# Kernel optimization log

Hardware: AMD Instinct MI355X
Metric: run time of the kernel (lower is better)

Reference implementation:

```python
import jax, jax.numpy as jnp
import numpy as np

H = 8          # num_heads
T = 2          # num_edge_types
NEG_SLOPE = 0.2


def _edge_softmax(scores, dst, num_nodes):
    # softmax over incoming edges of each destination node, per head
    m = jax.ops.segment_max(scores, dst, num_segments=num_nodes)  # [N,H]
    e = jnp.exp(scores - m[dst])                                   # [E,H]
    s = jax.ops.segment_sum(e, dst, num_segments=num_nodes)        # [N,H]
    return e / s[dst]


def setup_inputs() -> dict:
    key = jax.random.key(0)
    ks = jax.random.split(key, 8)
    N, D, E = 50000, 128, 800000
    return {
        "x": jax.random.normal(ks[0], (N, D), dtype=jnp.float32),
        "w_u": jax.random.normal(ks[1], (H * T, D), dtype=jnp.float32) * (1.0 / np.sqrt(D)),
        "b_u": jax.random.normal(ks[2], (H * T,), dtype=jnp.float32) * 0.01,
        "w_v": jax.random.normal(ks[3], (H * T, D), dtype=jnp.float32) * (1.0 / np.sqrt(D)),
        "src_e0": jax.random.randint(ks[4], (E,), 0, N, dtype=jnp.int32),
        "dst_e0": jax.random.randint(ks[5], (E,), 0, N, dtype=jnp.int32),
        "src_e1": jax.random.randint(ks[6], (E,), 0, N, dtype=jnp.int32),
        "dst_e1": jax.random.randint(ks[7], (E,), 0, N, dtype=jnp.int32),
    }


def reference(x, w_u, b_u, w_v, src_e0, dst_e0, src_e1, dst_e1):
    N, D = x.shape
    head_dim = D // H
    scores_u = x @ w_u.T + b_u   # [N, H*T]
    scores_v = x @ w_v.T         # [N, H*T]
    xh = x.reshape(N, head_dim, H)  # matches torch reshape(-1, head_dim, num_heads)
    outs = [x]  # sep=True
    for t, (src, dst) in enumerate([(src_e0, dst_e0), (src_e1, dst_e1)]):
        u = scores_u[:, t * H:(t + 1) * H]
        v = scores_v[:, t * H:(t + 1) * H]
        s = u[src] + v[dst]                         # u_add_v -> [E,H]
        s = jnp.where(s >= 0, s, NEG_SLOPE * s)     # LeakyReLU(0.2)
        p = _edge_softmax(s, dst, N)                # [E,H]
        msg = xh[src] * p[:, None, :]               # u_mul_e -> [E,head_dim,H]
        agg = jax.ops.segment_sum(msg, dst, num_segments=N)  # [N,head_dim,H]
        outs.append(agg.reshape(N, D))
    return jnp.concatenate(outs, axis=-1)  # [N, D*(1+T)]
```

## Files before the change

### kernel.cpp

```cpp
#include <hip/hip_runtime.h>

#define NEG_SLOPE 0.2f
#define RSHIFT 6
#define RW     64
#define MAXNR  800
#define CHUNKP 8192

__device__ __forceinline__ ushort f2bf(float f) {
    union { float f; unsigned u; } c; c.f = f;
    unsigned u = c.u;
    return (ushort)((u + 0x7fffu + ((u >> 16) & 1u)) >> 16);
}

__global__ __launch_bounds__(256) void mega_kernel(
    const float* __restrict__ x, const float* __restrict__ wu,
    const float* __restrict__ bu, const float* __restrict__ wv,
    const int* __restrict__ s0, const int* __restrict__ d0,
    const int* __restrict__ s1, const int* __restrict__ d1,
    float* __restrict__ out, ushort* __restrict__ xbf,
    float* __restrict__ su, float* __restrict__ sv,
    int* __restrict__ gcur, unsigned* __restrict__ pairs,
    int N, int E, int nr, int cap, int convBlocks, int scoreBlocks, int ppset)
{
    __shared__ float wlds[32 * 129];
    int* smi = (int*)wlds;
    int tid = threadIdx.x;
    int bid = blockIdx.x;

    if (bid < convBlocks) {
        int i = bid * 256 + tid;
        if (i < N * 32) {
            float4 v = ((const float4*)x)[i];
            int n = i >> 5, q = i & 31;
            ((float4*)out)[(size_t)n * 96 + q] = v;
            ushort4 b;
            b.x = f2bf(v.x); b.y = f2bf(v.y); b.z = f2bf(v.z); b.w = f2bf(v.w);
            *(ushort4*)(xbf + (size_t)i * 4) = b;
        }
        return;
    }
    if (bid < convBlocks + scoreBlocks) {
        for (int i = tid; i < 4096; i += 256) {
            int o = i >> 7, k = i & 127;
            wlds[o * 129 + k] = (o < 16) ? wu[i] : wv[i - 2048];
        }
        __syncthreads();
        int o = tid & 15;
        int n = (bid - convBlocks) * 16 + (tid >> 4);
        if (n >= N) return;
        const float4* xr4 = (const float4*)(x + (size_t)n * 128);
        const float* wur = wlds + o * 129;
        const float* wvr = wlds + (16 + o) * 129;
        float au = 0.f, av = 0.f;
#pragma unroll
        for (int kk = 0; kk < 32; ++kk) {
            float4 xv = xr4[kk];
            int k = kk * 4;
            au = fmaf(xv.x, wur[k],     au);  av = fmaf(xv.x, wvr[k],     av);
            au = fmaf(xv.y, wur[k + 1], au);  av = fmaf(xv.y, wvr[k + 1], av);
            au = fmaf(xv.z, wur[k + 2], au);  av = fmaf(xv.z, wvr[k + 2], av);
            au = fmaf(xv.w, wur[k + 3], au);  av = fmaf(xv.w, wvr[k + 3], av);
        }
        su[n * 16 + o] = au + bu[o];
        sv[n * 16 + o] = av;
        return;
    }
    int pb = bid - convBlocks - scoreBlocks;
    int t = pb / ppset, c = pb % ppset;
    const int* ss = t ? s1 : s0;
    const int* dd = t ? d1 : d0;
    int beg = c * CHUNKP, end = min(E, beg + CHUNKP);
    int* lcnt = smi; int* gb = smi + MAXNR; int* lrun = smi + 2 * MAXNR;
    for (int i = tid; i < nr; i += 256) lcnt[i] = 0;
    __syncthreads();
    for (int e = beg + tid; e < end; e += 256)
        atomicAdd(&lcnt[dd[e] >> RSHIFT], 1);
    __syncthreads();
    for (int i = tid; i < nr; i += 256) {
        gb[i] = atomicAdd(&gcur[t * nr + i], lcnt[i]);
        lrun[i] = 0;
    }
    __syncthreads();
    unsigned* pt = pairs + (size_t)t * nr * cap;
    for (int e = beg + tid; e < end; e += 256) {
        int dst = dd[e], src = ss[e];
        int r = dst >> RSHIFT;
        int pos = atomicAdd(&lrun[r], 1);
        pt[(size_t)r * cap + gb[r] + pos] = ((unsigned)dst << 16) | (unsigned)src;
    }
}

__global__ __launch_bounds__(256, 8) void buildagg_kernel(
    const ushort* __restrict__ xbf, const float* __restrict__ su,
    const float* __restrict__ sv, const int* __restrict__ gcur,
    const unsigned* __restrict__ pairs, float* __restrict__ out,
    int N, int E, int nr, int cap)
{
    __shared__ ushort srcs[1408];
    __shared__ int offl[65];
    __shared__ int cursor[64];
    __shared__ __align__(16) float ev4[4][512];
    int r = blockIdx.x, t = blockIdx.y, tid = threadIdx.x;
    int m = gcur[t * nr + r];
    if (m > cap) m = cap;
    const unsigned* p = pairs + ((size_t)t * nr + r) * cap;

    if (tid < 64) cursor[tid] = 0;
    __syncthreads();
    for (int i = tid; i < m; i += 256)
        atomicAdd(&cursor[(p[i] >> 16) & (RW - 1)], 1);
    __syncthreads();
    if (tid < 64) {
        int v = cursor[tid];
        int incl = v;
#pragma unroll
        for (int d = 1; d < 64; d <<= 1) {
            int o = __shfl(incl, tid - d);
            if (tid >= d) incl += o;
        }
        offl[tid + 1] = incl;
        if (tid == 0) offl[0] = 0;
        cursor[tid] = incl - v;
    }
    __syncthreads();
    for (int i = tid; i < m; i += 256) {
        unsigned v = p[i];
        int pos = atomicAdd(&cursor[(v >> 16) & (RW - 1)], 1);
        srcs[pos] = (ushort)(v & 0xffffu);
    }
    __syncthreads();

    int wid = tid >> 6, lane = tid & 63;
    int h = lane & 7, e8 = lane >> 3;
    int hf = lane >> 5, q = lane & 31;
    int j0 = q * 4, hbase = (q & 1) * 4;
    float* ev = ev4[wid];
    for (int ln = wid; ln < RW; ln += 4) {
        int n = (r << RSHIFT) + ln;
        if (n >= N) break;
        int beg = offl[ln], end = offl[ln + 1];
        float vh = sv[n * 16 + t * 8 + h];
        float acc0 = 0.f, acc1 = 0.f, acc2 = 0.f, acc3 = 0.f;
        float l = 0.f;
        for (int cbeg = beg; cbeg < end; cbeg += 64) {
            int cnt = min(end - cbeg, 64);
            int gmax = (cnt + 7) >> 3;
            for (int g = 0; g < gmax; ++g) {
                int e = g * 8 + e8;
                bool valid = e < cnt;
                int srcv = srcs[cbeg + (valid ? e : 0)];
                float sc = su[srcv * 16 + t * 8 + h] + vh;
                sc = (sc >= 0.f) ? sc : NEG_SLOPE * sc;
                float ee = valid ? __expf(sc) : 0.f;
                l += ee;
                ev[e * 8 + h] = ee;
            }
            int pairs2 = (cnt + 1) >> 1;
            for (int i2 = 0; i2 < pairs2; ++i2) {
                int eidx = i2 * 2 + hf;
                int srcv = srcs[cbeg + ((eidx < cnt) ? eidx : 0)];
                float4 p4 = *(const float4*)(ev + eidx * 8 + hbase);
                uint2 u = *(const uint2*)(xbf + (size_t)srcv * 128 + j0);
                float x0 = __uint_as_float(u.x << 16);
                float x1 = __uint_as_float(u.x & 0xffff0000u);
                float x2 = __uint_as_float(u.y << 16);
                float x3 = __uint_as_float(u.y & 0xffff0000u);
                acc0 = fmaf(x0, p4.x, acc0);
                acc1 = fmaf(x1, p4.y, acc1);
                acc2 = fmaf(x2, p4.z, acc2);
                acc3 = fmaf(x3, p4.w, acc3);
            }
        }
        l += __shfl_xor(l, 8);
        l += __shfl_xor(l, 16);
        l += __shfl_xor(l, 32);
        float invl = (l > 0.f) ? (1.f / l) : 0.f;
        acc0 += __shfl_xor(acc0, 32);
        acc1 += __shfl_xor(acc1, 32);
        acc2 += __shfl_xor(acc2, 32);
        acc3 += __shfl_xor(acc3, 32);
        float i0 = __shfl(invl, hbase);
        float i1 = __shfl(invl, hbase + 1);
        float i2v = __shfl(invl, hbase + 2);
        float i3 = __shfl(invl, hbase + 3);
        if (hf == 0) {
            float4 r4 = make_float4(acc0 * i0, acc1 * i1, acc2 * i2v, acc3 * i3);
            *(float4*)(out + (size_t)n * 384 + 128 + (size_t)t * 128 + j0) = r4;
        }
    }
}

extern "C" void kernel_launch(void* const* d_in, const int* in_sizes, int n_in,
                              void* d_out, int out_size, void* d_ws, size_t ws_size,
                              hipStream_t stream)
{
    const float* x  = (const float*)d_in[0];
    const float* wu = (const float*)d_in[1];
    const float* bu = (const float*)d_in[2];
    const float* wv = (const float*)d_in[3];
    const int* s0 = (const int*)d_in[4];
    const int* d0 = (const int*)d_in[5];
    const int* s1 = (const int*)d_in[6];
    const int* d1 = (const int*)d_in[7];
    float* out = (float*)d_out;
    int N = in_sizes[0] / 128;
    int E = in_sizes[4];

    int nr = ((N - 1) >> RSHIFT) + 1;
    long long mean = (long long)RW * E / N;
    int cap = (int)(mean + mean / 4 + 64);

    char* ws = (char*)d_ws;
    size_t o = 0;
    auto alloc = [&](size_t bytes) -> void* {
        void* p = ws + o;
        o = (o + bytes + 255) & ~(size_t)255;
        return p;
    };
    float* su       = (float*)alloc((size_t)N * 16 * 4);
    float* sv       = (float*)alloc((size_t)N * 16 * 4);
    int* gcur       = (int*)alloc((size_t)2 * nr * 4);
    unsigned* pairs = (unsigned*)alloc((size_t)2 * nr * cap * 4);
    ushort* xbf     = (ushort*)alloc((size_t)N * 128 * 2);

    int convBlocks  = (N * 32 + 255) / 256;
    int scoreBlocks = (N + 15) / 16;
    int ppset       = (E + CHUNKP - 1) / CHUNKP;

    hipMemsetAsync(gcur, 0, (size_t)2 * nr * 4, stream);
    mega_kernel<<<convBlocks + scoreBlocks + 2 * ppset, 256, 0, stream>>>(
        x, wu, bu, wv, s0, d0, s1, d1, out, xbf, su, sv,
        gcur, pairs, N, E, nr, cap, convBlocks, scoreBlocks, ppset);
    buildagg_kernel<<<dim3(nr, 2), 256, 0, stream>>>(
        xbf, su, sv, gcur, pairs, out, N, E, nr, cap);
}
```

Before: 262.3 us.

## Widen aggregation gathers to 16B per lane and reorder mega-kernel block roles

```diff
diff --git a/kernel.cpp b/kernel.cpp
--- a/kernel.cpp
+++ b/kernel.cpp
@@ -11,6 +11,8 @@
     unsigned u = c.u;
     return (ushort)((u + 0x7fffu + ((u >> 16) & 1u)) >> 16);
 }
+__device__ __forceinline__ float bflo(unsigned u) { return __uint_as_float(u << 16); }
+__device__ __forceinline__ float bfhi(unsigned u) { return __uint_as_float(u & 0xffff0000u); }
 
 __global__ __launch_bounds__(256) void mega_kernel(
     const float* __restrict__ x, const float* __restrict__ wu,
@@ -27,8 +29,34 @@
     int tid = threadIdx.x;
     int bid = blockIdx.x;
 
-    if (bid < convBlocks) {
-        int i = bid * 256 + tid;
+    if (bid < 2 * ppset) {
+        int pb = bid;
+        int t = pb / ppset, c = pb % ppset;
+        const int* ss = t ? s1 : s0;
+        const int* dd = t ? d1 : d0;
+        int beg = c * CHUNKP, end = min(E, beg + CHUNKP);
+        int* lcnt = smi; int* gb = smi + MAXNR; int* lrun = smi + 2 * MAXNR;
+        for (int i = tid; i < nr; i += 256) lcnt[i] = 0;
+        __syncthreads();
+        for (int e = beg + tid; e < end; e += 256)
+            atomicAdd(&lcnt[dd[e] >> RSHIFT], 1);
+        __syncthreads();
+        for (int i = tid; i < nr; i += 256) {
+            gb[i] = atomicAdd(&gcur[t * nr + i], lcnt[i]);
+            lrun[i] = 0;
+        }
+        __syncthreads();
+        unsigned* pt = pairs + (size_t)t * nr * cap;
+        for (int e = beg + tid; e < end; e += 256) {
+            int dst = dd[e], src = ss[e];
+            int rr = dst >> RSHIFT;
+            int pos = atomicAdd(&lrun[rr], 1);
+            pt[(size_t)rr * cap + gb[rr] + pos] = ((unsigned)dst << 16) | (unsigned)src;
+        }
+        return;
+    }
+    if (bid < 2 * ppset + convBlocks) {
+        int i = (bid - 2 * ppset) * 256 + tid;
         if (i < N * 32) {
             float4 v = ((const float4*)x)[i];
             int n = i >> 5, q = i & 31;
@@ -39,55 +67,29 @@
         }
         return;
     }
-    if (bid < convBlocks + scoreBlocks) {
-        for (int i = tid; i < 4096; i += 256) {
-            int o = i >> 7, k = i & 127;
-            wlds[o * 129 + k] = (o < 16) ? wu[i] : wv[i - 2048];
-        }
-        __syncthreads();
-        int o = tid & 15;
-        int n = (bid - convBlocks) * 16 + (tid >> 4);
-        if (n >= N) return;
-        const float4* xr4 = (const float4*)(x + (size_t)n * 128);
-        const float* wur = wlds + o * 129;
-        const float* wvr = wlds + (16 + o) * 129;
-        float au = 0.f, av = 0.f;
+    for (int i = tid; i < 4096; i += 256) {
+        int o = i >> 7, k = i & 127;
+        wlds[o * 129 + k] = (o < 16) ? wu[i] : wv[i - 2048];
+    }
+    __syncthreads();
+    int o = tid & 15;
+    int n = (bid - 2 * ppset - convBlocks) * 16 + (tid >> 4);
+    if (n >= N) return;
+    const float4* xr4 = (const float4*)(x + (size_t)n * 128);
+    const float* wur = wlds + o * 129;
+    const float* wvr = wlds + (16 + o) * 129;
+    float au = 0.f, av = 0.f;
 #pragma unroll
-        for (int kk = 0; kk < 32; ++kk) {
-            float4 xv = xr4[kk];
-            int k = kk * 4;
-            au = fmaf(xv.x, wur[k],     au);  av = fmaf(xv.x, wvr[k],     av);
-            au = fmaf(xv.y, wur[k + 1], au);  av = fmaf(xv.y, wvr[k + 1], av);
-            au = fmaf(xv.z, wur[k + 2], au);  av = fmaf(xv.z, wvr[k + 2], av);
-            au = fmaf(xv.w, wur[k + 3], au);  av = fmaf(xv.w, wvr[k + 3], av);
-        }
-        su[n * 16 + o] = au + bu[o];
-        sv[n * 16 + o] = av;
-        return;
-    }
-    int pb = bid - convBlocks - scoreBlocks;
-    int t = pb / ppset, c = pb % ppset;
-    const int* ss = t ? s1 : s0;
-    const int* dd = t ? d1 : d0;
-    int beg = c * CHUNKP, end = min(E, beg + CHUNKP);
-    int* lcnt = smi; int* gb = smi + MAXNR; int* lrun = smi + 2 * MAXNR;
-    for (int i = tid; i < nr; i += 256) lcnt[i] = 0;
-    __syncthreads();
-    for (int e = beg + tid; e < end; e += 256)
-        atomicAdd(&lcnt[dd[e] >> RSHIFT], 1);
-    __syncthreads();
-    for (int i = tid; i < nr; i += 256) {
-        gb[i] = atomicAdd(&gcur[t * nr + i], lcnt[i]);
-        lrun[i] = 0;
-    }
-    __syncthreads();
-    unsigned* pt = pairs + (size_t)t * nr * cap;
-    for (int e = beg + tid; e < end; e += 256) {
-        int dst = dd[e], src = ss[e];
-        int r = dst >> RSHIFT;
-        int pos = atomicAdd(&lrun[r], 1);
-        pt[(size_t)r * cap + gb[r] + pos] = ((unsigned)dst << 16) | (unsigned)src;
-    }
+    for (int kk = 0; kk < 32; ++kk) {
+        float4 xv = xr4[kk];
+        int k = kk * 4;
+        au = fmaf(xv.x, wur[k],     au);  av = fmaf(xv.x, wvr[k],     av);
+        au = fmaf(xv.y, wur[k + 1], au);  av = fmaf(xv.y, wvr[k + 1], av);
+        au = fmaf(xv.z, wur[k + 2], au);  av = fmaf(xv.z, wvr[k + 2], av);
+        au = fmaf(xv.w, wur[k + 3], au);  av = fmaf(xv.w, wvr[k + 3], av);
+    }
+    su[n * 16 + o] = au + bu[o];
+    sv[n * 16 + o] = av;
 }
 
 __global__ __launch_bounds__(256, 8) void buildagg_kernel(
@@ -132,60 +134,90 @@
 
     int wid = tid >> 6, lane = tid & 63;
     int h = lane & 7, e8 = lane >> 3;
-    int hf = lane >> 5, q = lane & 31;
-    int j0 = q * 4, hbase = (q & 1) * 4;
+    int g2 = lane >> 4, q16 = lane & 15;
+    int j0 = q16 * 8;
     float* ev = ev4[wid];
     for (int ln = wid; ln < RW; ln += 4) {
         int n = (r << RSHIFT) + ln;
         if (n >= N) break;
         int beg = offl[ln], end = offl[ln + 1];
         float vh = sv[n * 16 + t * 8 + h];
-        float acc0 = 0.f, acc1 = 0.f, acc2 = 0.f, acc3 = 0.f;
+        float a0 = 0.f, a1 = 0.f, a2 = 0.f, a3 = 0.f;
+        float a4 = 0.f, a5 = 0.f, a6 = 0.f, a7 = 0.f;
         float l = 0.f;
         for (int cbeg = beg; cbeg < end; cbeg += 64) {
             int cnt = min(end - cbeg, 64);
             int gmax = (cnt + 7) >> 3;
-            for (int g = 0; g < gmax; ++g) {
-                int e = g * 8 + e8;
-                bool valid = e < cnt;
-                int srcv = srcs[cbeg + (valid ? e : 0)];
-                float sc = su[srcv * 16 + t * 8 + h] + vh;
-                sc = (sc >= 0.f) ? sc : NEG_SLOPE * sc;
-                float ee = valid ? __expf(sc) : 0.f;
-                l += ee;
-                ev[e * 8 + h] = ee;
+            for (int g = 0; g < gmax; g += 2) {
+                int ea = g * 8 + e8, eb = ea + 8;
+                int sa = srcs[cbeg + ((ea < cnt) ? ea : 0)];
+                int sb = srcs[cbeg + ((eb < cnt) ? eb : 0)];
+                float fa = su[sa * 16 + t * 8 + h];
+                float fb = su[sb * 16 + t * 8 + h];
+                float sca = fa + vh;
+                float scb = fb + vh;
+                sca = (sca >= 0.f) ? sca : NEG_SLOPE * sca;
+                scb = (scb >= 0.f) ? scb : NEG_SLOPE * scb;
+                float eea = (ea < cnt) ? __expf(sca) : 0.f;
+                float eeb = (eb < cnt) ? __expf(scb) : 0.f;
+                l += eea;
+                l += eeb;
+                ev[ea * 8 + h] = eea;
+                ev[eb * 8 + h] = eeb;
             }
-            int pairs2 = (cnt + 1) >> 1;
-            for (int i2 = 0; i2 < pairs2; ++i2) {
-                int eidx = i2 * 2 + hf;
-                int srcv = srcs[cbeg + ((eidx < cnt) ? eidx : 0)];
-                float4 p4 = *(const float4*)(ev + eidx * 8 + hbase);
-                uint2 u = *(const uint2*)(xbf + (size_t)srcv * 128 + j0);
-                float x0 = __uint_as_float(u.x << 16);
-                float x1 = __uint_as_float(u.x & 0xffff0000u);
-                float x2 = __uint_as_float(u.y << 16);
-                float x3 = __uint_as_float(u.y & 0xffff0000u);
-                acc0 = fmaf(x0, p4.x, acc0);
-                acc1 = fmaf(x1, p4.y, acc1);
-                acc2 = fmaf(x2, p4.z, acc2);
-                acc3 = fmaf(x3, p4.w, acc3);
+            int quads = (cnt + 3) >> 2;
+            for (int i4 = 0; i4 < quads; i4 += 2) {
+                int e0 = (i4 << 2) + g2, e1 = e0 + 4;
+                int sA = srcs[cbeg + ((e0 < cnt) ? e0 : 0)];
+                int sB = srcs[cbeg + ((e1 < cnt) ? e1 : 0)];
+                uint4 uA = *(const uint4*)(xbf + (size_t)sA * 128 + j0);
+                uint4 uB = *(const uint4*)(xbf + (size_t)sB * 128 + j0);
+                float4 pA0 = *(const float4*)(ev + e0 * 8);
+                float4 pA1 = *(const float4*)(ev + e0 * 8 + 4);
+                float4 pB0 = *(const float4*)(ev + e1 * 8);
+                float4 pB1 = *(const float4*)(ev + e1 * 8 + 4);
+                a0 = fmaf(bflo(uA.x), pA0.x, a0);
+                a1 = fmaf(bfhi(uA.x), pA0.y, a1);
+                a2 = fmaf(bflo(uA.y), pA0.z, a2);
+                a3 = fmaf(bfhi(uA.y), pA0.w, a3);
+                a4 = fmaf(bflo(uA.z), pA1.x, a4);
+                a5 = fmaf(bfhi(uA.z), pA1.y, a5);
+                a6 = fmaf(bflo(uA.w), pA1.z, a6);
+                a7 = fmaf(bfhi(uA.w), pA1.w, a7);
+                a0 = fmaf(bflo(uB.x), pB0.x, a0);
+                a1 = fmaf(bfhi(uB.x), pB0.y, a1);
+                a2 = fmaf(bflo(uB.y), pB0.z, a2);
+                a3 = fmaf(bfhi(uB.y), pB0.w, a3);
+                a4 = fmaf(bflo(uB.z), pB1.x, a4);
+                a5 = fmaf(bfhi(uB.z), pB1.y, a5);
+                a6 = fmaf(bflo(uB.w), pB1.z, a6);
+                a7 = fmaf(bfhi(uB.w), pB1.w, a7);
             }
         }
         l += __shfl_xor(l, 8);
         l += __shfl_xor(l, 16);
         l += __shfl_xor(l, 32);
         float invl = (l > 0.f) ? (1.f / l) : 0.f;
-        acc0 += __shfl_xor(acc0, 32);
-        acc1 += __shfl_xor(acc1, 32);
-        acc2 += __shfl_xor(acc2, 32);
-        acc3 += __shfl_xor(acc3, 32);
-        float i0 = __shfl(invl, hbase);
-        float i1 = __shfl(invl, hbase + 1);
-        float i2v = __shfl(invl, hbase + 2);
-        float i3 = __shfl(invl, hbase + 3);
-        if (hf == 0) {
-            float4 r4 = make_float4(acc0 * i0, acc1 * i1, acc2 * i2v, acc3 * i3);
-            *(float4*)(out + (size_t)n * 384 + 128 + (size_t)t * 128 + j0) = r4;
+        a0 += __shfl_xor(a0, 16); a0 += __shfl_xor(a0, 32);
+        a1 += __shfl_xor(a1, 16); a1 += __shfl_xor(a1, 32);
+        a2 += __shfl_xor(a2, 16); a2 += __shfl_xor(a2, 32);
+        a3 += __shfl_xor(a3, 16); a3 += __shfl_xor(a3, 32);
+        a4 += __shfl_xor(a4, 16); a4 += __shfl_xor(a4, 32);
+        a5 += __shfl_xor(a5, 16); a5 += __shfl_xor(a5, 32);
+        a6 += __shfl_xor(a6, 16); a6 += __shfl_xor(a6, 32);
+        a7 += __shfl_xor(a7, 16); a7 += __shfl_xor(a7, 32);
+        float ih0 = __shfl(invl, 0);
+        float ih1 = __shfl(invl, 1);
+        float ih2 = __shfl(invl, 2);
+        float ih3 = __shfl(invl, 3);
+        float ih4 = __shfl(invl, 4);
+        float ih5 = __shfl(invl, 5);
+        float ih6 = __shfl(invl, 6);
+        float ih7 = __shfl(invl, 7);
+        if (g2 == 0) {
+            float* op = out + (size_t)n * 384 + 128 + (size_t)t * 128 + j0;
+            *(float4*)op       = make_float4(a0 * ih0, a1 * ih1, a2 * ih2, a3 * ih3);
+            *(float4*)(op + 4) = make_float4(a4 * ih4, a5 * ih5, a6 * ih6, a7 * ih7);
         }
     }
 }
```

Result: faster. 234.6 us (-10.6%).
